# Optimization experiments

Measured on AMD Instinct MI355X. Metric: run time of the kernel, lower is better.

The kernel has to match this reference:

```python
import jax, jax.numpy as jnp
import numpy as np

H = 8          # num heads
D = 16         # head dim
HID = 128      # hidden_dim = H * D
NM, ND, NA = 100000, 20000, 50000
E = 300000     # edges per relation
NUM_CLASSES = 8


def setup_inputs() -> dict:
    key = jax.random.key(0)
    ks = jax.random.split(key, 24)
    s = 0.05
    eye = jnp.eye(D, dtype=jnp.float32)
    inp = {
        'x_movie': jax.random.normal(ks[0], (NM, 256), jnp.float32),
        'x_director': jax.random.normal(ks[1], (ND, 128), jnp.float32),
        'x_actor': jax.random.normal(ks[2], (NA, 128), jnp.float32),
        # edge lists per relation: (director->movie, actor->movie, movie->director, movie->actor)
        'src_dm': jax.random.randint(ks[3], (E,), 0, ND),
        'dst_dm': jax.random.randint(ks[4], (E,), 0, NM),
        'src_am': jax.random.randint(ks[5], (E,), 0, NA),
        'dst_am': jax.random.randint(ks[6], (E,), 0, NM),
        'src_md': jax.random.randint(ks[7], (E,), 0, NM),
        'dst_md': jax.random.randint(ks[8], (E,), 0, ND),
        'src_ma': jax.random.randint(ks[9], (E,), 0, NM),
        'dst_ma': jax.random.randint(ks[10], (E,), 0, NA),
        # per-type pre-encoder (use_pre_encoder=True)
        'Wpre_m': jax.random.normal(ks[11], (256, HID), jnp.float32) * s,
        'Wpre_d': jax.random.normal(ks[12], (128, HID), jnp.float32) * s,
        'Wpre_a': jax.random.normal(ks[13], (128, HID), jnp.float32) * s,
        'bpre': jnp.zeros((3, HID), jnp.float32),
        # per-type K/Q/V projections, stacked over the 3 node types
        'Wk': jax.random.normal(ks[14], (3, HID, HID), jnp.float32) * s,
        'bk': jnp.zeros((3, HID), jnp.float32),
        'Wq': jax.random.normal(ks[15], (3, HID, HID), jnp.float32) * s,
        'bq': jnp.zeros((3, HID), jnp.float32),
        'Wv': jax.random.normal(ks[16], (3, HID, HID), jnp.float32) * s,
        'bv': jnp.zeros((3, HID), jnp.float32),
        # per-relation attention / message matrices and priors (4 relations)
        'a_rel': eye + jax.random.normal(ks[17], (4, H, D, D), jnp.float32) * s,
        'm_rel': eye + jax.random.normal(ks[18], (4, H, D, D), jnp.float32) * s,
        'p_rel': jnp.ones((4, H), jnp.float32),
        # per-type skip gate and output projection
        'skip': jnp.ones((3,), jnp.float32),
        'Wa': jax.random.normal(ks[19], (3, HID, HID), jnp.float32) * s,
        'ba': jnp.zeros((3, HID), jnp.float32),
        # final classification head on target node type ('movie')
        'Wlin': jax.random.normal(ks[20], (HID, NUM_CLASSES), jnp.float32) * s,
        'blin': jnp.zeros((NUM_CLASSES,), jnp.float32),
    }
    return inp


def _seg_softmax_agg(alpha, msg, dst, n):
    # softmax over incoming edges of each destination node, then weighted sum of msgs
    m = jax.ops.segment_max(alpha, dst, num_segments=n)      # [n, H]
    m = jnp.where(jnp.isfinite(m), m, 0.0)
    a = jnp.exp(alpha - m[dst])                              # [E, H]
    denom = jax.ops.segment_sum(a, dst, num_segments=n)      # [n, H]
    num = jax.ops.segment_sum(a[:, :, None] * msg, dst, num_segments=n)  # [n, H, D]
    return num / jnp.maximum(denom, 1e-16)[:, :, None]


def reference(x_movie, x_director, x_actor,
              src_dm, dst_dm, src_am, dst_am, src_md, dst_md, src_ma, dst_ma,
              Wpre_m, Wpre_d, Wpre_a, bpre, Wk, bk, Wq, bq, Wv, bv,
              a_rel, m_rel, p_rel, skip, Wa, ba, Wlin, blin):
    # type order: 0=movie, 1=director, 2=actor
    xs = [x_movie @ Wpre_m + bpre[0],
          x_director @ Wpre_d + bpre[1],
          x_actor @ Wpre_a + bpre[2]]
    k = [(x @ Wk[t] + bk[t]).reshape(-1, H, D) for t, x in enumerate(xs)]
    q = [(x @ Wq[t] + bq[t]).reshape(-1, H, D) for t, x in enumerate(xs)]
    v = [(x @ Wv[t] + bv[t]).reshape(-1, H, D) for t, x in enumerate(xs)]

    # (src_type, dst_type, src_idx, dst_idx) per relation
    rels = [(1, 0, src_dm, dst_dm), (2, 0, src_am, dst_am),
            (0, 1, src_md, dst_md), (0, 2, src_ma, dst_ma)]
    scale = 1.0 / np.sqrt(D).astype(np.float32)
    buckets = {0: [], 1: [], 2: []}
    for r, (st, dt, src, dst) in enumerate(rels):
        ke = jnp.einsum('ehd,hdf->ehf', k[st][src], a_rel[r])          # [E,H,D]
        al = jnp.einsum('ehf,ehf->eh', q[dt][dst], ke) * p_rel[r] * scale
        me = jnp.einsum('ehd,hdf->ehf', v[st][src], m_rel[r])          # [E,H,D]
        buckets[dt].append((al, me, dst))

    n = [x.shape[0] for x in xs]
    outs = []
    for t in range(3):
        al = jnp.concatenate([b[0] for b in buckets[t]], axis=0)
        me = jnp.concatenate([b[1] for b in buckets[t]], axis=0)
        dst = jnp.concatenate([b[2] for b in buckets[t]], axis=0)
        agg = _seg_softmax_agg(al, me, dst, n[t]).reshape(n[t], HID)
        h = jax.nn.gelu(agg, approximate=False) @ Wa[t] + ba[t]
        g = jax.nn.sigmoid(skip[t])
        outs.append(g * h + (1.0 - g) * xs[t])

    return outs[0] @ Wlin + blin
```

## Files before the change

kernel.cpp:

```cpp
#include <hip/hip_runtime.h>
#include <hip/hip_bf16.h>
#include <math.h>

#define NM 100000
#define ND 20000
#define NA 50000
#define EDG 300000
#define CAP 32

typedef __attribute__((ext_vector_type(8))) short shortx8;
typedef __attribute__((ext_vector_type(4))) float floatx4;
typedef __attribute__((ext_vector_type(4))) int intx4;

__device__ __forceinline__ float bf2f(unsigned int u) {
    return __uint_as_float(u << 16);
}
__device__ __forceinline__ unsigned short f2bf(float f) {
    unsigned int x = __float_as_uint(f);
    unsigned int r = x + 0x7fffu + ((x >> 16) & 1u);
    return (unsigned short)(r >> 16);
}
__device__ __forceinline__ unsigned short f2bf_fast(float f) {
    return (unsigned short)((__float_as_uint(f) + 0x8000u) >> 16);
}
__device__ __forceinline__ unsigned int pkbf2(float a, float b) {
    return __builtin_amdgcn_perm(__float_as_uint(b) + 0x8000u,
                                 __float_as_uint(a) + 0x8000u,
                                 0x07060302u);
}
__device__ __forceinline__ float gelu_exact(float x) {
    return 0.5f * x * (1.0f + erff(x * 0.70710678118654752f));
}

static const size_t OFF_BT_Q      = 0;
static const size_t OFF_BT_KAMV_D = 73728;
static const size_t OFF_BT_KAMV_A = 139264;
static const size_t OFF_WKA_D     = 204800;
static const size_t OFF_WVM_D     = 270336;
static const size_t OFF_WKA_A     = 335872;
static const size_t OFF_WVM_A     = 401408;
static const size_t OFF_BQ        = 466944;
static const size_t OFF_B_KAMV_D  = 467520;
static const size_t OFF_B_KAMV_A  = 468544;
static const size_t OFF_BKA_D     = 469568;
static const size_t OFF_BVM_D     = 470080;
static const size_t OFF_BKA_A     = 470592;
static const size_t OFF_BVM_A     = 471104;
static const size_t OFF_WALS      = 471616;
static const size_t OFF_BFIN      = 475712;
static const size_t OFF_Q0        = 524288;
static const size_t OFF_SKIPB     = 26124288;
static const size_t OFF_KAMV_D    = 29324288;
static const size_t OFF_KAMV_A    = 39564288;
static const size_t OFF_COUNTS    = 65164288;
static const size_t OFF_SLOTS     = 65564288;
#define KAMV_A_DELTA 10240000

__global__ __launch_bounds__(256) void precompA(
    const float* __restrict__ Wk, const float* __restrict__ bk,
    const float* __restrict__ Wv, const float* __restrict__ bv,
    const float* __restrict__ Wa, const float* __restrict__ ba,
    const float* __restrict__ Wlin, const float* __restrict__ blin,
    const float* __restrict__ a_rel, const float* __restrict__ m_rel,
    const float* __restrict__ p_rel, const float* __restrict__ skip,
    const float* __restrict__ bpre,
    char* __restrict__ ws)
{
    int tid = blockIdx.x * 256 + threadIdx.x;
    if (tid < 65536) {
        int mat = tid >> 14, rem = tid & 16383;
        int e = rem >> 7, hf = rem & 127, h = hf >> 4, f = hf & 15;
        const float* Wsrc; const float* R; float sc; float* dst;
        if (mat == 0)      { Wsrc = Wk + 16384; R = a_rel;        sc = p_rel[h]     * 0.25f; dst = (float*)(ws + OFF_WKA_D); }
        else if (mat == 1) { Wsrc = Wv + 16384; R = m_rel;        sc = 1.0f;                 dst = (float*)(ws + OFF_WVM_D); }
        else if (mat == 2) { Wsrc = Wk + 32768; R = a_rel + 2048; sc = p_rel[8 + h] * 0.25f; dst = (float*)(ws + OFF_WKA_A); }
        else               { Wsrc = Wv + 32768; R = m_rel + 2048; sc = 1.0f;                 dst = (float*)(ws + OFF_WVM_A); }
        float s = 0.0f;
        for (int d = 0; d < 16; d++)
            s += Wsrc[e * 128 + h * 16 + d] * R[h * 256 + d * 16 + f];
        dst[e * 128 + hf] = s * sc;
    } else if (tid < 66048) {
        int idx = tid - 65536;
        int mat = idx >> 7, hf = idx & 127, h = hf >> 4, f = hf & 15;
        const float* bsrc; const float* R; float sc; float* dst;
        if (mat == 0)      { bsrc = bk + 128; R = a_rel;        sc = p_rel[h]     * 0.25f; dst = (float*)(ws + OFF_BKA_D); }
        else if (mat == 1) { bsrc = bv + 128; R = m_rel;        sc = 1.0f;                 dst = (float*)(ws + OFF_BVM_D); }
        else if (mat == 2) { bsrc = bk + 256; R = a_rel + 2048; sc = p_rel[8 + h] * 0.25f; dst = (float*)(ws + OFF_BKA_A); }
        else               { bsrc = bv + 256; R = m_rel + 2048; sc = 1.0f;                 dst = (float*)(ws + OFF_BVM_A); }
        float s = 0.0f;
        for (int d = 0; d < 16; d++)
            s += bsrc[h * 16 + d] * R[h * 256 + d * 16 + f];
        dst[hf] = s * sc;
    } else if (tid < 67072) {
        int idx = tid - 66048;
        int j = idx >> 3, c = idx & 7;
        float g = 1.0f / (1.0f + __expf(-skip[0]));
        float s = 0.0f;
        for (int o = 0; o < 128; o++)
            s += Wa[j * 128 + o] * Wlin[o * 8 + c];
        ((float*)(ws + OFF_WALS))[j * 8 + c] = g * s;
    } else if (tid < 67080) {
        int c = tid - 67072;
        float g = 1.0f / (1.0f + __expf(-skip[0]));
        float s1 = 0.0f, s2 = 0.0f;
        for (int o = 0; o < 128; o++) {
            s1 += ba[o]   * Wlin[o * 8 + c];
            s2 += bpre[o] * Wlin[o * 8 + c];
        }
        ((float*)(ws + OFF_BFIN))[c] = g * s1 + (1.0f - g) * s2 + blin[c];
    } else if (tid < 67080 + NM) {
        ((int*)(ws + OFF_COUNTS))[tid - 67080] = 0;
    }
}

__global__ __launch_bounds__(256) void precompB(
    const float* __restrict__ Wpre_m, const float* __restrict__ Wpre_d,
    const float* __restrict__ Wpre_a, const float* __restrict__ bpre,
    const float* __restrict__ Wq, const float* __restrict__ bq,
    const float* __restrict__ Wlin, const float* __restrict__ skip,
    char* __restrict__ ws)
{
    int tid = blockIdx.x * 256 + threadIdx.x;
    const float* WKA_D = (const float*)(ws + OFF_WKA_D);
    const float* WVM_D = (const float*)(ws + OFF_WVM_D);
    const float* WKA_A = (const float*)(ws + OFF_WKA_A);
    const float* WVM_A = (const float*)(ws + OFF_WVM_A);

    if (tid < 36864) {
        int n = tid >> 8, c = tid & 255;
        float s = 0.0f;
        if (n < 128) {
            for (int e = 0; e < 128; e++)
                s += Wpre_m[c * 128 + e] * Wq[e * 128 + n];
        } else if (n < 136) {
            int cc = n - 128;
            float g = 1.0f / (1.0f + __expf(-skip[0]));
            for (int e = 0; e < 128; e++)
                s += Wpre_m[c * 128 + e] * Wlin[e * 8 + cc];
            s *= (1.0f - g);
        }
        ((unsigned short*)(ws + OFF_BT_Q))[n * 256 + c] = f2bf(s);
    } else if (tid < 69632) {
        int idx = tid - 36864;
        int nrow = idx >> 7, c = idx & 127;
        const float* Wf = (nrow < 128) ? WKA_D : WVM_D;
        int nc = nrow & 127;
        float s = 0.0f;
        for (int e = 0; e < 128; e++)
            s += Wpre_d[c * 128 + e] * Wf[e * 128 + nc];
        ((unsigned short*)(ws + OFF_BT_KAMV_D))[nrow * 128 + c] = f2bf(s);
    } else if (tid < 102400) {
        int idx = tid - 69632;
        int nrow = idx >> 7, c = idx & 127;
        const float* Wf = (nrow < 128) ? WKA_A : WVM_A;
        int nc = nrow & 127;
        float s = 0.0f;
        for (int e = 0; e < 128; e++)
            s += Wpre_a[c * 128 + e] * Wf[e * 128 + nc];
        ((unsigned short*)(ws + OFF_BT_KAMV_A))[nrow * 128 + c] = f2bf(s);
    } else if (tid < 102544) {
        int n = tid - 102400;
        float s = 0.0f;
        if (n < 128) {
            for (int e = 0; e < 128; e++)
                s += bpre[e] * Wq[e * 128 + n];
            s += bq[n];
        }
        ((float*)(ws + OFF_BQ))[n] = s;
    } else if (tid < 102800) {
        int nrow = tid - 102544;
        const float* Wf  = (nrow < 128) ? WKA_D : WVM_D;
        const float* bf_ = (nrow < 128) ? (const float*)(ws + OFF_BKA_D) : (const float*)(ws + OFF_BVM_D);
        int nc = nrow & 127;
        float s = 0.0f;
        for (int e = 0; e < 128; e++)
            s += bpre[128 + e] * Wf[e * 128 + nc];
        ((float*)(ws + OFF_B_KAMV_D))[nrow] = s + bf_[nc];
    } else if (tid < 103056) {
        int nrow = tid - 102800;
        const float* Wf  = (nrow < 128) ? WKA_A : WVM_A;
        const float* bf_ = (nrow < 128) ? (const float*)(ws + OFF_BKA_A) : (const float*)(ws + OFF_BVM_A);
        int nc = nrow & 127;
        float s = 0.0f;
        for (int e = 0; e < 128; e++)
            s += bpre[256 + e] * Wf[e * 128 + nc];
        ((float*)(ws + OFF_B_KAMV_A))[nrow] = s + bf_[nc];
    }
}

__global__ __launch_bounds__(256) void edge_scatter(
    const int* __restrict__ src_dm, const int* __restrict__ dst_dm,
    const int* __restrict__ src_am, const int* __restrict__ dst_am,
    int* __restrict__ counts, int* __restrict__ slots)
{
    int t = blockIdx.x * 256 + threadIdx.x;
    if (t >= 2 * EDG) return;
    int src, dst, delta;
    if (t < EDG) { src = src_dm[t];       dst = dst_dm[t];       delta = 0; }
    else         { src = src_am[t - EDG]; dst = dst_am[t - EDG]; delta = KAMV_A_DELTA; }
    int pos = atomicAdd(&counts[dst], 1);
    if (pos < CAP) slots[(size_t)dst * CAP + pos] = src * 512 + delta;
}

#define MFMA16(a, b, c) __builtin_amdgcn_mfma_f32_16x16x32_bf16(a, b, c, 0, 0, 0)

template<int K, int NT, bool SKIP>
__global__ __launch_bounds__(256) void gemm_bt(
    const float* __restrict__ A, int M,
    const unsigned short* __restrict__ BT,
    const float* __restrict__ bias,
    unsigned short* __restrict__ outb, int ldout,
    float* __restrict__ skipb)
{
    __shared__ unsigned short blds[NT * 16 * 136];
    int tid = threadIdx.x;
    int w = tid >> 6, lane = tid & 63;
    int quad = lane >> 4, low = lane & 15;
    int rbase = blockIdx.x * 128 + w * 32;

    floatx4 acc[2][NT] = {};
    int rows[2];
    #pragma unroll
    for (int mt = 0; mt < 2; mt++) {
        int m = rbase + mt * 16 + low;
        if (m >= M) m = M - 1;
        rows[mt] = m;
    }

    constexpr int HALVES = K / 128;
    for (int hfi = 0; hfi < HALVES; hfi++) {
        if (hfi) __syncthreads();
        for (int idx = tid; idx < NT * 16 * 16; idx += 256) {
            int n = idx >> 4, ch = idx & 15;
            *(intx4*)(&blds[n * 136 + ch * 8]) =
                *(const intx4*)(&BT[(size_t)n * K + hfi * 128 + ch * 8]);
        }
        __syncthreads();

        #pragma unroll
        for (int ks = 0; ks < 4; ks++) {
            int ko = hfi * 128 + ks * 32 + quad * 8;
            shortx8 afr[2];
            #pragma unroll
            for (int mt = 0; mt < 2; mt++) {
                const float* ap = A + (size_t)rows[mt] * K + ko;
                floatx4 f0 = *(const floatx4*)ap;
                floatx4 f1 = *(const floatx4*)(ap + 4);
                union { intx4 i4; shortx8 s8; } av;
                av.i4[0] = (int)pkbf2(f0[0], f0[1]);
                av.i4[1] = (int)pkbf2(f0[2], f0[3]);
                av.i4[2] = (int)pkbf2(f1[0], f1[1]);
                av.i4[3] = (int)pkbf2(f1[2], f1[3]);
                afr[mt] = av.s8;
            }
            #pragma unroll
            for (int nt = 0; nt < NT; nt++) {
                shortx8 b = *(const shortx8*)(&blds[(nt * 16 + low) * 136 + ks * 32 + quad * 8]);
                acc[0][nt] = MFMA16(afr[0], b, acc[0][nt]);
                acc[1][nt] = MFMA16(afr[1], b, acc[1][nt]);
            }
        }
    }

    #pragma unroll
    for (int mt = 0; mt < 2; mt++) {
        #pragma unroll
        for (int nt = 0; nt < NT; nt++) {
            #pragma unroll
            for (int r = 0; r < 4; r++) {
                int row = rbase + mt * 16 + quad * 4 + r;
                if (row >= M) continue;
                int col = nt * 16 + low;
                float v = acc[mt][nt][r] + bias[col];
                if (SKIP && nt == 8) {
                    if (low < 8) skipb[(size_t)row * 8 + low] = v;
                } else {
                    outb[(size_t)row * ldout + col] = f2bf_fast(v);
                }
            }
        }
    }
}

__global__ __launch_bounds__(256, 2) void gemm_kamv(
    const float* __restrict__ A_d, const float* __restrict__ A_a,
    const unsigned short* __restrict__ BT_d, const unsigned short* __restrict__ BT_a,
    const float* __restrict__ bias_d, const float* __restrict__ bias_a,
    unsigned short* __restrict__ out_d, unsigned short* __restrict__ out_a)
{
    __shared__ unsigned short blds[256 * 136];
    const int NBLK_D = (ND + 127) / 128;
    bool isD = (int)blockIdx.x < NBLK_D;
    const float* A            = isD ? A_d    : A_a;
    const unsigned short* BT  = isD ? BT_d   : BT_a;
    const float* bias         = isD ? bias_d : bias_a;
    unsigned short* outb      = isD ? out_d  : out_a;
    int M  = isD ? ND : NA;
    int bx = isD ? (int)blockIdx.x : (int)blockIdx.x - NBLK_D;

    int tid = threadIdx.x;
    int w = tid >> 6, lane = tid & 63;
    int quad = lane >> 4, low = lane & 15;
    int rbase = bx * 128 + w * 32;

    for (int idx = tid; idx < 256 * 16; idx += 256) {
        int n = idx >> 4, ch = idx & 15;
        *(intx4*)(&blds[n * 136 + ch * 8]) =
            *(const intx4*)(&BT[(size_t)n * 128 + ch * 8]);
    }

    floatx4 acc[2][16] = {};
    int rows[2];
    #pragma unroll
    for (int mt = 0; mt < 2; mt++) {
        int m = rbase + mt * 16 + low;
        if (m >= M) m = M - 1;
        rows[mt] = m;
    }
    __syncthreads();

    #pragma unroll
    for (int ks = 0; ks < 4; ks++) {
        int ko = ks * 32 + quad * 8;
        shortx8 afr[2];
        #pragma unroll
        for (int mt = 0; mt < 2; mt++) {
            const float* ap = A + (size_t)rows[mt] * 128 + ko;
            floatx4 f0 = *(const floatx4*)ap;
            floatx4 f1 = *(const floatx4*)(ap + 4);
            union { intx4 i4; shortx8 s8; } av;
            av.i4[0] = (int)pkbf2(f0[0], f0[1]);
            av.i4[1] = (int)pkbf2(f0[2], f0[3]);
            av.i4[2] = (int)pkbf2(f1[0], f1[1]);
            av.i4[3] = (int)pkbf2(f1[2], f1[3]);
            afr[mt] = av.s8;
        }
        #pragma unroll
        for (int nt = 0; nt < 16; nt++) {
            shortx8 b = *(const shortx8*)(&blds[(nt * 16 + low) * 136 + ko]);
            acc[0][nt] = MFMA16(afr[0], b, acc[0][nt]);
            acc[1][nt] = MFMA16(afr[1], b, acc[1][nt]);
        }
    }

    #pragma unroll
    for (int mt = 0; mt < 2; mt++) {
        #pragma unroll
        for (int nt = 0; nt < 16; nt++) {
            #pragma unroll
            for (int r = 0; r < 4; r++) {
                int row = rbase + mt * 16 + quad * 4 + r;
                if (row >= M) continue;
                int col = nt * 16 + low;
                outb[(size_t)row * 256 + col] = f2bf_fast(acc[mt][nt][r] + bias[col]);
            }
        }
    }
}

__global__ __launch_bounds__(256) void agg_kernel(
    const unsigned short* __restrict__ q0,
    const char* __restrict__ kamv0,
    const int* __restrict__ counts, const int* __restrict__ slots,
    const float* __restrict__ skipb,
    const float* __restrict__ WaLs, const float* __restrict__ bfin,
    float* __restrict__ out)
{
    __shared__ float wals[1032];
    for (int i = threadIdx.x; i < 1024; i += 256) {
        int c = i >> 7, rem = i & 127, j = rem >> 4, L = rem & 15;
        wals[i] = WaLs[(L * 8 + j) * 8 + c];
    }
    if (threadIdx.x < 8) wals[1024 + threadIdx.x] = bfin[threadIdx.x];
    __syncthreads();

    int lane = threadIdx.x & 63;
    int grp = lane >> 4;
    int L   = lane & 15;
    int n = blockIdx.x * 16 + (threadIdx.x >> 6) * 4 + grp;

    intx4 qv = *(const intx4*)(q0 + (size_t)n * 128 + L * 8);
    float qf[8];
    #pragma unroll
    for (int d = 0; d < 4; d++) {
        unsigned int u = (unsigned int)qv[d];
        qf[2 * d]     = __uint_as_float(u << 16);
        qf[2 * d + 1] = __uint_as_float(u & 0xffff0000u);
    }

    int cnt = counts[n];
    cnt = cnt < 0 ? 0 : (cnt > CAP ? CAP : cnt);
    int s0 = slots[(size_t)n * CAP + L];

    float acc[8] = {0, 0, 0, 0, 0, 0, 0, 0};
    float den = 0.0f;
    for (int i = 0; i < cnt; i++) {
        int off = __shfl(s0, (lane & 48) + (i & 15));
        if (__builtin_expect(i >= 16, 0)) off = slots[(size_t)n * CAP + i];
        const char* p = kamv0 + off;
        intx4 ku = *(const intx4*)(p + L * 16);
        intx4 mu = *(const intx4*)(p + 256 + L * 16);
        float ph = 0.0f;
        #pragma unroll
        for (int d = 0; d < 4; d++) {
            unsigned int u = (unsigned int)ku[d];
            ph += qf[2 * d]     * __uint_as_float(u << 16);
            ph += qf[2 * d + 1] * __uint_as_float(u & 0xffff0000u);
        }
        float pf = ph + __shfl_xor(ph, 1);
        float wgt = __expf(fminf(pf, 60.0f));
        den += wgt;
        #pragma unroll
        for (int d = 0; d < 4; d++) {
            unsigned int u = (unsigned int)mu[d];
            acc[2 * d]     += wgt * __uint_as_float(u << 16);
            acc[2 * d + 1] += wgt * __uint_as_float(u & 0xffff0000u);
        }
    }
    float inv = 1.0f / fmaxf(den, 1e-16f);

    float part[8] = {0, 0, 0, 0, 0, 0, 0, 0};
    #pragma unroll
    for (int j = 0; j < 8; j++) {
        float u = gelu_exact(acc[j] * inv);
        #pragma unroll
        for (int c = 0; c < 8; c++)
            part[c] += u * wals[c * 128 + j * 16 + L];
    }

    bool b0 = lane & 1, b1 = lane & 2, b2 = lane & 4;
    float t1[4], t2[2], t3;
    #pragma unroll
    for (int k = 0; k < 4; k++) {
        float send = b0 ? part[k] : part[4 + k];
        float got  = __shfl_xor(send, 1);
        t1[k] = (b0 ? part[4 + k] : part[k]) + got;
    }
    #pragma unroll
    for (int k = 0; k < 2; k++) {
        float send = b1 ? t1[k] : t1[2 + k];
        float got  = __shfl_xor(send, 2);
        t2[k] = (b1 ? t1[2 + k] : t1[k]) + got;
    }
    {
        float send = b2 ? t2[0] : t2[1];
        float got  = __shfl_xor(send, 4);
        t3 = (b2 ? t2[1] : t2[0]) + got;
    }
    t3 += __shfl_xor(t3, 8);
    if (L < 8) {
        int c = 4 * (L & 1) + 2 * ((L >> 1) & 1) + ((L >> 2) & 1);
        out[(size_t)n * 8 + c] = t3 + skipb[(size_t)n * 8 + c] + wals[1024 + c];
    }
}

extern "C" void kernel_launch(void* const* d_in, const int* in_sizes, int n_in,
                              void* d_out, int out_size, void* d_ws, size_t ws_size,
                              hipStream_t stream) {
    (void)in_sizes; (void)n_in; (void)out_size; (void)ws_size;
    const float* x_movie    = (const float*)d_in[0];
    const float* x_director = (const float*)d_in[1];
    const float* x_actor    = (const float*)d_in[2];
    const int* src_dm = (const int*)d_in[3];
    const int* dst_dm = (const int*)d_in[4];
    const int* src_am = (const int*)d_in[5];
    const int* dst_am = (const int*)d_in[6];
    const float* Wpre_m = (const float*)d_in[11];
    const float* Wpre_d = (const float*)d_in[12];
    const float* Wpre_a = (const float*)d_in[13];
    const float* bpre   = (const float*)d_in[14];
    const float* Wk     = (const float*)d_in[15];
    const float* bk     = (const float*)d_in[16];
    const float* Wq     = (const float*)d_in[17];
    const float* bq     = (const float*)d_in[18];
    const float* Wv     = (const float*)d_in[19];
    const float* bv     = (const float*)d_in[20];
    const float* a_rel  = (const float*)d_in[21];
    const float* m_rel  = (const float*)d_in[22];
    const float* p_rel  = (const float*)d_in[23];
    const float* skip   = (const float*)d_in[24];
    const float* Wa     = (const float*)d_in[25];
    const float* ba     = (const float*)d_in[26];
    const float* Wlin   = (const float*)d_in[27];
    const float* blin   = (const float*)d_in[28];

    char* ws = (char*)d_ws;
    float* out = (float*)d_out;

    precompA<<<(67080 + NM + 255) / 256, 256, 0, stream>>>(
        Wk, bk, Wv, bv, Wa, ba, Wlin, blin,
        a_rel, m_rel, p_rel, skip, bpre, ws);
    precompB<<<403, 256, 0, stream>>>(Wpre_m, Wpre_d, Wpre_a, bpre,
                                      Wq, bq, Wlin, skip, ws);

    edge_scatter<<<(2 * EDG + 255) / 256, 256, 0, stream>>>(
        src_dm, dst_dm, src_am, dst_am,
        (int*)(ws + OFF_COUNTS), (int*)(ws + OFF_SLOTS));

    gemm_bt<256, 9, true><<<(NM + 127) / 128, 256, 0, stream>>>(
        x_movie, NM, (const unsigned short*)(ws + OFF_BT_Q),
        (const float*)(ws + OFF_BQ),
        (unsigned short*)(ws + OFF_Q0), 128, (float*)(ws + OFF_SKIPB));

    gemm_kamv<<<(ND + 127) / 128 + (NA + 127) / 128, 256, 0, stream>>>(
        x_director, x_actor,
        (const unsigned short*)(ws + OFF_BT_KAMV_D),
        (const unsigned short*)(ws + OFF_BT_KAMV_A),
        (const float*)(ws + OFF_B_KAMV_D), (const float*)(ws + OFF_B_KAMV_A),
        (unsigned short*)(ws + OFF_KAMV_D), (unsigned short*)(ws + OFF_KAMV_A));

    agg_kernel<<<NM / 16, 256, 0, stream>>>(
        (const unsigned short*)(ws + OFF_Q0),
        (const char*)(ws + OFF_KAMV_D),
        (const int*)(ws + OFF_COUNTS), (const int*)(ws + OFF_SLOTS),
        (const float*)(ws + OFF_SKIPB),
        (const float*)(ws + OFF_WALS), (const float*)(ws + OFF_BFIN), out);
}
```

Before: 439.8 us.

## Stage A tiles in LDS with coalesced loads and split kamv GEMM columns

Both GEMMs now load the fp32 A tile cooperatively with coalesced row-major reads, convert it to bf16 once and stage it in LDS. Before, each wave read A fragments straight from global memory in an MFMA-fragment pattern. The kamv GEMM is also split along a second grid dimension into two 128-column halves. This halves LDS and accumulator registers per block and doubles the block count, at the cost of reading and converting A twice. The movie GEMM gains a launch bound of 2 blocks per CU and extra LDS for the A tile.

After: 446.9 us. No clear change (+1.6%).

```diff
diff --git a/kernel.cpp b/kernel.cpp
--- a/kernel.cpp
+++ b/kernel.cpp
@@ -204,60 +204,51 @@
 
 #define MFMA16(a, b, c) __builtin_amdgcn_mfma_f32_16x16x32_bf16(a, b, c, 0, 0, 0)
 
-template<int K, int NT, bool SKIP>
-__global__ __launch_bounds__(256) void gemm_bt(
+template<int NT, bool SKIP>
+__global__ __launch_bounds__(256, 2) void gemm_m(
     const float* __restrict__ A, int M,
     const unsigned short* __restrict__ BT,
     const float* __restrict__ bias,
     unsigned short* __restrict__ outb, int ldout,
     float* __restrict__ skipb)
 {
-    __shared__ unsigned short blds[NT * 16 * 136];
+    __shared__ unsigned short a_lds[128 * 136];
+    __shared__ unsigned short b_lds[NT * 16 * 136];
     int tid = threadIdx.x;
     int w = tid >> 6, lane = tid & 63;
     int quad = lane >> 4, low = lane & 15;
     int rbase = blockIdx.x * 128 + w * 32;
 
     floatx4 acc[2][NT] = {};
-    int rows[2];
-    #pragma unroll
-    for (int mt = 0; mt < 2; mt++) {
-        int m = rbase + mt * 16 + low;
-        if (m >= M) m = M - 1;
-        rows[mt] = m;
-    }
-
-    constexpr int HALVES = K / 128;
-    for (int hfi = 0; hfi < HALVES; hfi++) {
+
+    for (int hfi = 0; hfi < 2; hfi++) {
         if (hfi) __syncthreads();
         for (int idx = tid; idx < NT * 16 * 16; idx += 256) {
             int n = idx >> 4, ch = idx & 15;
-            *(intx4*)(&blds[n * 136 + ch * 8]) =
-                *(const intx4*)(&BT[(size_t)n * K + hfi * 128 + ch * 8]);
+            *(intx4*)(&b_lds[n * 136 + ch * 8]) =
+                *(const intx4*)(&BT[(size_t)n * 256 + hfi * 128 + ch * 8]);
+        }
+        for (int f = tid; f < 4096; f += 256) {
+            int r = f >> 5, c4 = f & 31;
+            int rg = blockIdx.x * 128 + r;
+            if (rg >= M) rg = M - 1;
+            floatx4 v = *(const floatx4*)(A + (size_t)rg * 256 + hfi * 128 + c4 * 4);
+            unsigned long long d =
+                ((unsigned long long)pkbf2(v[2], v[3]) << 32) | pkbf2(v[0], v[1]);
+            *(unsigned long long*)(&a_lds[r * 136 + c4 * 4]) = d;
         }
         __syncthreads();
 
         #pragma unroll
         for (int ks = 0; ks < 4; ks++) {
-            int ko = hfi * 128 + ks * 32 + quad * 8;
-            shortx8 afr[2];
-            #pragma unroll
-            for (int mt = 0; mt < 2; mt++) {
-                const float* ap = A + (size_t)rows[mt] * K + ko;
-                floatx4 f0 = *(const floatx4*)ap;
-                floatx4 f1 = *(const floatx4*)(ap + 4);
-                union { intx4 i4; shortx8 s8; } av;
-                av.i4[0] = (int)pkbf2(f0[0], f0[1]);
-                av.i4[1] = (int)pkbf2(f0[2], f0[3]);
-                av.i4[2] = (int)pkbf2(f1[0], f1[1]);
-                av.i4[3] = (int)pkbf2(f1[2], f1[3]);
-                afr[mt] = av.s8;
-            }
+            int ko = ks * 32 + quad * 8;
+            shortx8 a0 = *(const shortx8*)(&a_lds[(w * 32 + low) * 136 + ko]);
+            shortx8 a1 = *(const shortx8*)(&a_lds[(w * 32 + 16 + low) * 136 + ko]);
             #pragma unroll
             for (int nt = 0; nt < NT; nt++) {
-                shortx8 b = *(const shortx8*)(&blds[(nt * 16 + low) * 136 + ks * 32 + quad * 8]);
-                acc[0][nt] = MFMA16(afr[0], b, acc[0][nt]);
-                acc[1][nt] = MFMA16(afr[1], b, acc[1][nt]);
+                shortx8 b = *(const shortx8*)(&b_lds[(nt * 16 + low) * 136 + ko]);
+                acc[0][nt] = MFMA16(a0, b, acc[0][nt]);
+                acc[1][nt] = MFMA16(a1, b, acc[1][nt]);
             }
         }
     }
@@ -288,71 +279,63 @@
     const float* __restrict__ bias_d, const float* __restrict__ bias_a,
     unsigned short* __restrict__ out_d, unsigned short* __restrict__ out_a)
 {
-    __shared__ unsigned short blds[256 * 136];
+    __shared__ unsigned short a_lds[128 * 136];
+    __shared__ unsigned short b_lds[128 * 136];
     const int NBLK_D = (ND + 127) / 128;
     bool isD = (int)blockIdx.x < NBLK_D;
-    const float* A            = isD ? A_d    : A_a;
-    const unsigned short* BT  = isD ? BT_d   : BT_a;
-    const float* bias         = isD ? bias_d : bias_a;
-    unsigned short* outb      = isD ? out_d  : out_a;
+    const float* A           = isD ? A_d    : A_a;
+    const unsigned short* BT = (isD ? BT_d : BT_a) + (size_t)blockIdx.y * 128 * 128;
+    const float* bias        = (isD ? bias_d : bias_a) + blockIdx.y * 128;
+    unsigned short* outb     = isD ? out_d  : out_a;
     int M  = isD ? ND : NA;
     int bx = isD ? (int)blockIdx.x : (int)blockIdx.x - NBLK_D;
+    int col_off = blockIdx.y * 128;
 
     int tid = threadIdx.x;
     int w = tid >> 6, lane = tid & 63;
     int quad = lane >> 4, low = lane & 15;
     int rbase = bx * 128 + w * 32;
 
-    for (int idx = tid; idx < 256 * 16; idx += 256) {
+    for (int idx = tid; idx < 2048; idx += 256) {
         int n = idx >> 4, ch = idx & 15;
-        *(intx4*)(&blds[n * 136 + ch * 8]) =
+        *(intx4*)(&b_lds[n * 136 + ch * 8]) =
             *(const intx4*)(&BT[(size_t)n * 128 + ch * 8]);
     }
-
-    floatx4 acc[2][16] = {};
-    int rows[2];
-    #pragma unroll
-    for (int mt = 0; mt < 2; mt++) {
-        int m = rbase + mt * 16 + low;
-        if (m >= M) m = M - 1;
-        rows[mt] = m;
+    for (int f = tid; f < 4096; f += 256) {
+        int r = f >> 5, c4 = f & 31;
+        int rg = bx * 128 + r;
+        if (rg >= M) rg = M - 1;
+        floatx4 v = *(const floatx4*)(A + (size_t)rg * 128 + c4 * 4);
+        unsigned long long d =
+            ((unsigned long long)pkbf2(v[2], v[3]) << 32) | pkbf2(v[0], v[1]);
+        *(unsigned long long*)(&a_lds[r * 136 + c4 * 4]) = d;
     }
     __syncthreads();
 
+    floatx4 acc[2][8] = {};
     #pragma unroll
     for (int ks = 0; ks < 4; ks++) {
         int ko = ks * 32 + quad * 8;
-        shortx8 afr[2];
-        #pragma unroll
-        for (int mt = 0; mt < 2; mt++) {
-            const float* ap = A + (size_t)rows[mt] * 128 + ko;
-            floatx4 f0 = *(const floatx4*)ap;
-            floatx4 f1 = *(const floatx4*)(ap + 4);
-            union { intx4 i4; shortx8 s8; } av;
-            av.i4[0] = (int)pkbf2(f0[0], f0[1]);
-            av.i4[1] = (int)pkbf2(f0[2], f0[3]);
-            av.i4[2] = (int)pkbf2(f1[0], f1[1]);
-            av.i4[3] = (int)pkbf2(f1[2], f1[3]);
-            afr[mt] = av.s8;
-        }
-        #pragma unroll
-        for (int nt = 0; nt < 16; nt++) {
-            shortx8 b = *(const shortx8*)(&blds[(nt * 16 + low) * 136 + ko]);
-            acc[0][nt] = MFMA16(afr[0], b, acc[0][nt]);
-            acc[1][nt] = MFMA16(afr[1], b, acc[1][nt]);
+        shortx8 a0 = *(const shortx8*)(&a_lds[(w * 32 + low) * 136 + ko]);
+        shortx8 a1 = *(const shortx8*)(&a_lds[(w * 32 + 16 + low) * 136 + ko]);
+        #pragma unroll
+        for (int nt = 0; nt < 8; nt++) {
+            shortx8 b = *(const shortx8*)(&b_lds[(nt * 16 + low) * 136 + ko]);
+            acc[0][nt] = MFMA16(a0, b, acc[0][nt]);
+            acc[1][nt] = MFMA16(a1, b, acc[1][nt]);
         }
     }
 
     #pragma unroll
     for (int mt = 0; mt < 2; mt++) {
         #pragma unroll
-        for (int nt = 0; nt < 16; nt++) {
+        for (int nt = 0; nt < 8; nt++) {
             #pragma unroll
             for (int r = 0; r < 4; r++) {
                 int row = rbase + mt * 16 + quad * 4 + r;
                 if (row >= M) continue;
                 int col = nt * 16 + low;
-                outb[(size_t)row * 256 + col] = f2bf_fast(acc[mt][nt][r] + bias[col]);
+                outb[(size_t)row * 256 + col_off + col] = f2bf_fast(acc[mt][nt][r] + bias[col]);
             }
         }
     }
@@ -497,12 +480,12 @@
         src_dm, dst_dm, src_am, dst_am,
         (int*)(ws + OFF_COUNTS), (int*)(ws + OFF_SLOTS));
 
-    gemm_bt<256, 9, true><<<(NM + 127) / 128, 256, 0, stream>>>(
+    gemm_m<9, true><<<(NM + 127) / 128, 256, 0, stream>>>(
         x_movie, NM, (const unsigned short*)(ws + OFF_BT_Q),
         (const float*)(ws + OFF_BQ),
         (unsigned short*)(ws + OFF_Q0), 128, (float*)(ws + OFF_SKIPB));
 
-    gemm_kamv<<<(ND + 127) / 128 + (NA + 127) / 128, 256, 0, stream>>>(
+    gemm_kamv<<<dim3((ND + 127) / 128 + (NA + 127) / 128, 2), 256, 0, stream>>>(
         x_director, x_actor,
         (const unsigned short*)(ws + OFF_BT_KAMV_D),
         (const unsigned short*)(ws + OFF_BT_KAMV_A),
```
